# Performance work log

Measured on AMD Instinct MI355X. Metric: run time of the kernel, lower is better.

Reference implementation:

```python
import jax, jax.numpy as jnp
import numpy as np

T, H = 2048, 2048          # tokens, hidden_size
E, I = 16, 768             # num_experts, moe_intermediate_size
K = 2                      # top_k


def setup_inputs() -> dict:
    key = jax.random.key(0)
    k1, k2, k3, k4, k5 = jax.random.split(key, 5)
    hidden_states = jax.random.normal(k1, (T, H), dtype=jnp.float32)
    top_k_index = jax.random.randint(k2, (T, K), 0, E, dtype=jnp.int64)
    top_k_weights = jax.random.uniform(k3, (T, K), dtype=jnp.float32)
    gate_up_proj = jax.random.normal(k4, (E, 2 * I, H), dtype=jnp.float32) * 0.02
    down_proj = jax.random.normal(k5, (E, H, I), dtype=jnp.float32) * 0.02
    return {
        "hidden_states": hidden_states,
        "top_k_index": top_k_index,
        "top_k_weights": top_k_weights,
        "gate_up_proj": gate_up_proj,
        "down_proj": down_proj,
    }


def reference(hidden_states, top_k_index, top_k_weights, gate_up_proj, down_proj):
    # Dense combine-weight matrix C[t, e] = sum of routing weights of token t for expert e.
    # Scatter-add matches index_add_ semantics (duplicate expert picks sum their weights,
    # which equals the eager per-(token, k) accumulation since the expert FFN is the same).
    t_idx = jnp.arange(hidden_states.shape[0])[:, None]
    C = jnp.zeros((hidden_states.shape[0], gate_up_proj.shape[0]), dtype=hidden_states.dtype)
    C = C.at[t_idx, top_k_index].add(top_k_weights.astype(hidden_states.dtype))

    inter = down_proj.shape[2]
    # [T, E, 2I]: each expert's gate_up GEMM applied to every token (zero-weight tokens
    # contribute nothing after combining with C).
    gu = jnp.einsum("th,eoh->teo", hidden_states, gate_up_proj)
    gate, up = gu[..., :inter], gu[..., inter:]
    h = jax.nn.silu(gate) * up                      # [T, E, I]
    y = jnp.einsum("tei,ehi->teh", h, down_proj)    # [T, E, H]
    return jnp.einsum("teh,te->th", y, C)           # weighted combine -> [T, H]
```

## Files before the change

kernel.cpp:

```cpp
#include <hip/hip_runtime.h>
#include <hip/hip_bf16.h>
#include <cstdint>
#include <cstddef>

#define T_TOK 2048
#define HID   2048
#define NEXP  16
#define INTER 768
#define TOPK  2
#define CAP   1024
#define MBLK  8

using short8  = __attribute__((ext_vector_type(8))) short;
using f32x16  = __attribute__((ext_vector_type(16))) float;

#define MFMA(a,b,c) __builtin_amdgcn_mfma_f32_32x32x16_bf16((a),(b),(c),0,0,0)

__device__ inline ushort bf16h(float x) {
    union { __hip_bfloat16 b; ushort u; } cv; cv.b = __float2bfloat16(x); return cv.u;
}
__device__ inline void split8(float4 a, float4 b, short8& h, short8& l) {
    float v[8] = {a.x,a.y,a.z,a.w,b.x,b.y,b.z,b.w};
    #pragma unroll
    for (int j = 0; j < 8; ++j) {
        ushort hb = bf16h(v[j]);
        float hf = __uint_as_float(((uint32_t)hb) << 16);
        h[j] = (short)hb;
        l[j] = (short)bf16h(v[j] - hf);
    }
}

__global__ __launch_bounds__(256)
void route_kernel(const int* __restrict__ idx, const float* __restrict__ wts,
                  int* __restrict__ counts, int* __restrict__ pair_tk,
                  float* __restrict__ pair_w) {
    int p = blockIdx.x * blockDim.x + threadIdx.x;
    if (p >= T_TOK * TOPK) return;
    int e = idx[p];
    int pos = atomicAdd(&counts[e], 1);
    if (pos < CAP) {
        pair_tk[e * CAP + pos] = p;
        pair_w [e * CAP + pos] = wts[p];
    }
}

__global__ __launch_bounds__(256)
void stage1_kernel(const float* __restrict__ hs, const float* __restrict__ gup,
                   const int* __restrict__ counts, const int* __restrict__ pair_tk,
                   float* __restrict__ gu) {
    __shared__ ushort Ahi[4*512], Alo[4*512];
    __shared__ ushort Bhi[16*512], Blo[16*512];
    __shared__ int s_tk[64];

    const int e  = blockIdx.z >> 1;
    const int ks = blockIdx.z & 1;
    const int cnt = min(counts[e], CAP);
    const int m0  = blockIdx.y * 64;
    if (m0 >= cnt) return;
    const int n0  = blockIdx.x * 128;

    const int tid = threadIdx.x, lane = tid & 63, w = tid >> 6;
    if (tid < 64) s_tk[tid] = pair_tk[e*CAP + min(m0+tid, cnt-1)];
    __syncthreads();

    const int ar = tid & 63, aq = tid >> 6;
    const float* asrc = hs + (size_t)(s_tk[ar] >> 1)*HID + ks*1024 + aq*8;
    const int br = tid;
    const float* bsrc = gup + (size_t)e*(2*INTER)*HID
                      + (size_t)((br < 128) ? (n0+br) : (INTER + n0 + br - 128))*HID
                      + ks*1024;

    const int fA  = (ar>>5)*2 + (aq>>1);
    const int lnA = (ar&31) + 32*(aq&1);
    const int rgB = br >> 5, lnB = br & 31;

    f32x16 accg[2], accu[2];
    #pragma unroll
    for (int i=0;i<16;++i){ accg[0][i]=0.f; accg[1][i]=0.f; accu[0][i]=0.f; accu[1][i]=0.f; }

    float4 a0c,a1c,bvc[8], a0n,a1n,bvn[8];
    a0c = *(const float4*)(asrc + 0);
    a1c = *(const float4*)(asrc + 4);
    #pragma unroll
    for (int q=0;q<8;++q) bvc[q] = *(const float4*)(bsrc + 4*q);

#define S1_BODY(A0,A1,BV,A0N,A1N,BVN,KST)                                        \
    {                                                                            \
        __syncthreads();                                                         \
        { short8 h,l; split8(A0,A1,h,l);                                         \
          *(short8*)&Ahi[(fA<<9)+(lnA<<3)] = h;                                  \
          *(short8*)&Alo[(fA<<9)+(lnA<<3)] = l; }                                \
        _Pragma("unroll")                                                        \
        for (int o=0;o<4;++o) { short8 h,l; split8(BV[2*o],BV[2*o+1],h,l);       \
          int f = rgB*2 + (o>>1); int ln = lnB + 32*(o&1);                       \
          *(short8*)&Bhi[(f<<9)+(ln<<3)] = h;                                    \
          *(short8*)&Blo[(f<<9)+(ln<<3)] = l; }                                  \
        if ((KST)+1 < 32) {                                                      \
            int ko = ((KST)+1)*32;                                               \
            A0N = *(const float4*)(asrc + ko);                                   \
            A1N = *(const float4*)(asrc + ko + 4);                               \
            _Pragma("unroll")                                                    \
            for (int q=0;q<8;++q) BVN[q] = *(const float4*)(bsrc + ko + 4*q);    \
        }                                                                        \
        __syncthreads();                                                         \
        const int ro = lane << 3;                                                \
        _Pragma("unroll")                                                        \
        for (int kf=0;kf<2;++kf) {                                               \
            short8 ah0 = *(const short8*)&Ahi[((0*2+kf)<<9)+ro];                 \
            short8 ah1 = *(const short8*)&Ahi[((1*2+kf)<<9)+ro];                 \
            short8 al0 = *(const short8*)&Alo[((0*2+kf)<<9)+ro];                 \
            short8 al1 = *(const short8*)&Alo[((1*2+kf)<<9)+ro];                 \
            short8 bgh = *(const short8*)&Bhi[(((w  )*2+kf)<<9)+ro];             \
            short8 bgl = *(const short8*)&Blo[(((w  )*2+kf)<<9)+ro];             \
            short8 buh = *(const short8*)&Bhi[(((4+w)*2+kf)<<9)+ro];             \
            short8 bul = *(const short8*)&Blo[(((4+w)*2+kf)<<9)+ro];             \
            accg[0] = MFMA(ah0,bgh,accg[0]);                                     \
            accg[1] = MFMA(ah1,bgh,accg[1]);                                     \
            accu[0] = MFMA(ah0,buh,accu[0]);                                     \
            accu[1] = MFMA(ah1,buh,accu[1]);                                     \
            accg[0] = MFMA(al0,bgh,accg[0]);                                     \
            accg[1] = MFMA(al1,bgh,accg[1]);                                     \
            accu[0] = MFMA(al0,buh,accu[0]);                                     \
            accu[1] = MFMA(al1,buh,accu[1]);                                     \
            accg[0] = MFMA(ah0,bgl,accg[0]);                                     \
            accg[1] = MFMA(ah1,bgl,accg[1]);                                     \
            accu[0] = MFMA(ah0,bul,accu[0]);                                     \
            accu[1] = MFMA(ah1,bul,accu[1]);                                     \
        }                                                                        \
    }

    for (int kst = 0; kst < 32; kst += 2) {
        S1_BODY(a0c,a1c,bvc,a0n,a1n,bvn,kst)
        S1_BODY(a0n,a1n,bvn,a0c,a1c,bvc,kst+1)
    }
#undef S1_BODY

    const int crhi = (lane>>5)*4, cl = lane&31;
    const int colg = n0 + 32*w + cl;
    #pragma unroll
    for (int mi=0;mi<2;++mi)
      #pragma unroll
      for (int r=0;r<16;++r) {
        int row = mi*32 + (r&3) + 8*(r>>2) + crhi;
        if (m0 + row < cnt) {
            size_t base = (size_t)s_tk[row]*(2*INTER);
            atomicAdd(&gu[base + colg],         accg[mi][r]);
            atomicAdd(&gu[base + INTER + colg], accu[mi][r]);
        }
      }
}

__global__ __launch_bounds__(256)
void fuse_kernel(const float* __restrict__ gu, ushort* __restrict__ hhi,
                 ushort* __restrict__ hlo) {
    int id  = blockIdx.x*256 + threadIdx.x;
    int row = id / (INTER/4);
    int c4  = (id % (INTER/4)) * 4;
    const float* gr = gu + (size_t)row*(2*INTER) + c4;
    float4 g = *(const float4*)gr;
    float4 u = *(const float4*)(gr + INTER);
    float hv[4];
    hv[0] = g.x/(1.f+__expf(-g.x))*u.x;
    hv[1] = g.y/(1.f+__expf(-g.y))*u.y;
    hv[2] = g.z/(1.f+__expf(-g.z))*u.z;
    hv[3] = g.w/(1.f+__expf(-g.w))*u.w;
    ushort4 hh, hl;
    {
        ushort h0 = bf16h(hv[0]); float f0 = __uint_as_float(((uint32_t)h0)<<16);
        ushort h1 = bf16h(hv[1]); float f1 = __uint_as_float(((uint32_t)h1)<<16);
        ushort h2 = bf16h(hv[2]); float f2 = __uint_as_float(((uint32_t)h2)<<16);
        ushort h3 = bf16h(hv[3]); float f3 = __uint_as_float(((uint32_t)h3)<<16);
        hh = make_ushort4(h0,h1,h2,h3);
        hl = make_ushort4(bf16h(hv[0]-f0), bf16h(hv[1]-f1), bf16h(hv[2]-f2), bf16h(hv[3]-f3));
    }
    *(ushort4*)&hhi[(size_t)row*INTER + c4] = hh;
    *(ushort4*)&hlo[(size_t)row*INTER + c4] = hl;
}

__global__ __launch_bounds__(256)
void stage2_kernel(const ushort* __restrict__ hhi, const ushort* __restrict__ hlo,
                   const float* __restrict__ dwn, const int* __restrict__ counts,
                   const int* __restrict__ pair_tk, const float* __restrict__ pair_w,
                   float* __restrict__ out) {
    __shared__ ushort Ahi[4*512], Alo[4*512];
    __shared__ ushort Bhi[16*512], Blo[16*512];
    __shared__ int   s_tk[64];
    __shared__ float s_w[64];

    const int e  = blockIdx.z >> 1;
    const int ks = blockIdx.z & 1;
    const int cnt = min(counts[e], CAP);
    const int m0  = blockIdx.y * 64;
    if (m0 >= cnt) return;
    const int n0  = blockIdx.x * 256;

    const int tid = threadIdx.x, lane = tid & 63, w = tid >> 6;
    if (tid < 64) {
        int slot = min(m0+tid, cnt-1);
        s_tk[tid] = pair_tk[e*CAP + slot];
        s_w[tid]  = pair_w [e*CAP + slot];
    }
    __syncthreads();

    const int fA = tid >> 6, lnA = tid & 63;
    const int arow = (fA>>1)*32 + (lnA & 31);
    const int aoct = lnA >> 5, akf = fA & 1;
    const size_t aoff = (size_t)s_tk[arow]*INTER + ks*384 + akf*16 + aoct*8;
    const ushort* ahsrc = hhi + aoff;
    const ushort* alsrc = hlo + aoff;

    const int br = tid;
    const float* bsrc = dwn + (size_t)e*HID*INTER + (size_t)(n0+br)*INTER + ks*384;
    const int rgB = br >> 5, lnB = br & 31;

    f32x16 acc[2][2];
    #pragma unroll
    for (int mi=0;mi<2;++mi)
      #pragma unroll
      for (int ni=0;ni<2;++ni)
        #pragma unroll
        for (int i=0;i<16;++i) acc[mi][ni][i] = 0.f;

    short8 ahc, alc, ahn, aln;
    float4 bvc[8], bvn[8];
    ahc = *(const short8*)(ahsrc);
    alc = *(const short8*)(alsrc);
    #pragma unroll
    for (int q=0;q<8;++q) bvc[q] = *(const float4*)(bsrc + 4*q);

#define S2_BODY(AH,AL,BV,AHN,ALN,BVN,KST)                                        \
    {                                                                            \
        __syncthreads();                                                         \
        *(short8*)&Ahi[(fA<<9)+(lnA<<3)] = AH;                                   \
        *(short8*)&Alo[(fA<<9)+(lnA<<3)] = AL;                                   \
        _Pragma("unroll")                                                        \
        for (int o=0;o<4;++o) { short8 h,l; split8(BV[2*o],BV[2*o+1],h,l);       \
          int f = rgB*2 + (o>>1); int ln = lnB + 32*(o&1);                       \
          *(short8*)&Bhi[(f<<9)+(ln<<3)] = h;                                    \
          *(short8*)&Blo[(f<<9)+(ln<<3)] = l; }                                  \
        if ((KST)+1 < 12) {                                                      \
            int ko = ((KST)+1)*32;                                               \
            AHN = *(const short8*)(ahsrc + ko);                                  \
            ALN = *(const short8*)(alsrc + ko);                                  \
            _Pragma("unroll")                                                    \
            for (int q=0;q<8;++q) BVN[q] = *(const float4*)(bsrc + ko + 4*q);    \
        }                                                                        \
        __syncthreads();                                                         \
        const int ro = lane << 3;                                                \
        _Pragma("unroll")                                                        \
        for (int kf=0;kf<2;++kf) {                                               \
            short8 ah0 = *(const short8*)&Ahi[((0*2+kf)<<9)+ro];                 \
            short8 ah1 = *(const short8*)&Ahi[((1*2+kf)<<9)+ro];                 \
            short8 al0 = *(const short8*)&Alo[((0*2+kf)<<9)+ro];                 \
            short8 al1 = *(const short8*)&Alo[((1*2+kf)<<9)+ro];                 \
            _Pragma("unroll")                                                    \
            for (int ni=0;ni<2;++ni) {                                           \
                short8 bh = *(const short8*)&Bhi[(((2*w+ni)*2+kf)<<9)+ro];       \
                short8 bl = *(const short8*)&Blo[(((2*w+ni)*2+kf)<<9)+ro];       \
                acc[0][ni] = MFMA(ah0,bh,acc[0][ni]);                            \
                acc[1][ni] = MFMA(ah1,bh,acc[1][ni]);                            \
                acc[0][ni] = MFMA(al0,bh,acc[0][ni]);                            \
                acc[1][ni] = MFMA(al1,bh,acc[1][ni]);                            \
                acc[0][ni] = MFMA(ah0,bl,acc[0][ni]);                            \
                acc[1][ni] = MFMA(ah1,bl,acc[1][ni]);                            \
            }                                                                    \
        }                                                                        \
    }

    for (int kst = 0; kst < 12; kst += 2) {
        S2_BODY(ahc,alc,bvc,ahn,aln,bvn,kst)
        S2_BODY(ahn,aln,bvn,ahc,alc,bvc,kst+1)
    }
#undef S2_BODY

    const int crhi = (lane>>5)*4, cl = lane&31;
    #pragma unroll
    for (int mi=0;mi<2;++mi)
      #pragma unroll
      for (int r=0;r<16;++r) {
        int row = mi*32 + (r&3) + 8*(r>>2) + crhi;
        if (m0 + row < cnt) {
            int   t  = s_tk[row] >> 1;
            float wt = s_w[row];
            #pragma unroll
            for (int ni=0;ni<2;++ni) {
                int col = n0 + 64*w + 32*ni + cl;
                atomicAdd(&out[(size_t)t*HID + col], wt*acc[mi][ni][r]);
            }
        }
      }
}

extern "C" void kernel_launch(void* const* d_in, const int* in_sizes, int n_in,
                              void* d_out, int out_size, void* d_ws, size_t ws_size,
                              hipStream_t stream) {
    const float* hs  = (const float*)d_in[0];
    const int*   idx = (const int*)  d_in[1];
    const float* wts = (const float*)d_in[2];
    const float* gup = (const float*)d_in[3];
    const float* dwn = (const float*)d_in[4];
    float* out = (float*)d_out;

    char* ws = (char*)d_ws;
    int*    counts  = (int*)ws;
    int*    pair_tk = (int*)(ws + 1024);
    float*  pair_w  = (float*)(ws + 1024 + NEXP*CAP*4);
    float*  gu      = (float*)(ws + 262144);
    ushort* hhi     = (ushort*)(ws + 262144 + 25165824);
    ushort* hlo     = (ushort*)(ws + 262144 + 25165824 + 6291456);

    hipMemsetAsync(counts, 0, NEXP*sizeof(int), stream);
    hipMemsetAsync(gu, 0, (size_t)T_TOK*TOPK*2*INTER*sizeof(float), stream);
    hipMemsetAsync(out, 0, (size_t)T_TOK*HID*sizeof(float), stream);

    route_kernel<<<(T_TOK*TOPK + 255)/256, 256, 0, stream>>>(idx, wts, counts, pair_tk, pair_w);
    stage1_kernel<<<dim3(INTER/128, MBLK, NEXP*2), 256, 0, stream>>>(hs, gup, counts, pair_tk, gu);
    fuse_kernel<<<(T_TOK*TOPK*INTER/4)/256, 256, 0, stream>>>(gu, hhi, hlo);
    stage2_kernel<<<dim3(HID/256, MBLK, NEXP*2), 256, 0, stream>>>(hhi, hlo, dwn, counts, pair_tk, pair_w, out);
}
```

Before: 638.7 us.

## Pre-convert weights to bf16 and stream tiles via global_load_lds double buffering

Adds prep kernels that convert the expert weights to single bf16 and the hidden states to a hi/lo bf16 pair before the GEMMs. The grouped GEMMs then load ready-made bf16 tiles straight into double-buffered LDS with global_load_lds, which removes the per-tile register split and halves weight traffic. The block order is remapped and occupancy hints are added. Dropping the weight lo term cuts MFMA work by a third but lowers accuracy. The weights are re-converted on every call, which costs extra passes over memory. A fallback path is kept for when the workspace is too small.

Result: no change. 634.3 us (-0.7%).

```diff
diff --git a/kernel.cpp b/kernel.cpp
--- a/kernel.cpp
+++ b/kernel.cpp
@@ -18,6 +18,10 @@
 
 __device__ inline ushort bf16h(float x) {
     union { __hip_bfloat16 b; ushort u; } cv; cv.b = __float2bfloat16(x); return cv.u;
+}
+__device__ inline void gl16(const void* g, void* l) {
+    __builtin_amdgcn_global_load_lds((const __attribute__((address_space(1))) void*)g,
+                                     (__attribute__((address_space(3))) void*)l, 16, 0, 0);
 }
 __device__ inline void split8(float4 a, float4 b, short8& h, short8& l) {
     float v[8] = {a.x,a.y,a.z,a.w,b.x,b.y,b.z,b.w};
@@ -45,97 +49,94 @@
 }
 
 __global__ __launch_bounds__(256)
-void stage1_kernel(const float* __restrict__ hs, const float* __restrict__ gup,
-                   const int* __restrict__ counts, const int* __restrict__ pair_tk,
-                   float* __restrict__ gu) {
-    __shared__ ushort Ahi[4*512], Alo[4*512];
-    __shared__ ushort Bhi[16*512], Blo[16*512];
+void prep_bf16_kernel(const float4* __restrict__ src, ushort4* __restrict__ dst, int n4) {
+    int stride = gridDim.x * blockDim.x;
+    for (int i = blockIdx.x*blockDim.x + threadIdx.x; i < n4; i += stride) {
+        float4 v = src[i];
+        dst[i] = make_ushort4(bf16h(v.x), bf16h(v.y), bf16h(v.z), bf16h(v.w));
+    }
+}
+
+__global__ __launch_bounds__(256)
+void prep_hilo_kernel(const float4* __restrict__ src, ushort4* __restrict__ hi,
+                      ushort4* __restrict__ lo, int n4) {
+    int stride = gridDim.x * blockDim.x;
+    for (int i = blockIdx.x*blockDim.x + threadIdx.x; i < n4; i += stride) {
+        float4 v = src[i];
+        ushort h0=bf16h(v.x), h1=bf16h(v.y), h2=bf16h(v.z), h3=bf16h(v.w);
+        hi[i] = make_ushort4(h0,h1,h2,h3);
+        lo[i] = make_ushort4(bf16h(v.x - __uint_as_float((uint32_t)h0<<16)),
+                             bf16h(v.y - __uint_as_float((uint32_t)h1<<16)),
+                             bf16h(v.z - __uint_as_float((uint32_t)h2<<16)),
+                             bf16h(v.w - __uint_as_float((uint32_t)h3<<16)));
+    }
+}
+
+__global__ __launch_bounds__(256, 3)
+void s1mm_kernel(const ushort* __restrict__ hshi, const ushort* __restrict__ hslo,
+                 const ushort* __restrict__ gupb,
+                 const int* __restrict__ counts, const int* __restrict__ pair_tk,
+                 float* __restrict__ gu) {
+    __shared__ ushort Ab[2][8*512];
+    __shared__ ushort Bb[2][16*512];
     __shared__ int s_tk[64];
 
-    const int e  = blockIdx.z >> 1;
-    const int ks = blockIdx.z & 1;
+    const int lin  = blockIdx.x;
+    const int work = (lin & 7)*192 + (lin >> 3);
+    const int x = work % 6, y = (work/6) & 7, z = work/48;
+    const int e = z >> 1, ks = z & 1;
     const int cnt = min(counts[e], CAP);
-    const int m0  = blockIdx.y * 64;
+    const int m0 = y*64;
     if (m0 >= cnt) return;
-    const int n0  = blockIdx.x * 128;
-
-    const int tid = threadIdx.x, lane = tid & 63, w = tid >> 6;
+    const int n0 = x*128;
+
+    const int tid = threadIdx.x, ln = tid & 63, w = tid >> 6;
     if (tid < 64) s_tk[tid] = pair_tk[e*CAP + min(m0+tid, cnt-1)];
     __syncthreads();
 
-    const int ar = tid & 63, aq = tid >> 6;
-    const float* asrc = hs + (size_t)(s_tk[ar] >> 1)*HID + ks*1024 + aq*8;
-    const int br = tid;
-    const float* bsrc = gup + (size_t)e*(2*INTER)*HID
-                      + (size_t)((br < 128) ? (n0+br) : (INTER + n0 + br - 128))*HID
-                      + ks*1024;
-
-    const int fA  = (ar>>5)*2 + (aq>>1);
-    const int lnA = (ar&31) + 32*(aq&1);
-    const int rgB = br >> 5, lnB = br & 31;
+    const int lr = ln & 31, oc = (ln >> 5)*8;
+    const int tkA = s_tk[(w & 1)*32 + lr];
+    const ushort* hp = (w >> 1) ? hslo : hshi;
+    const ushort* aA = hp + (size_t)(tkA >> 1)*HID + ks*1024 + oc;
+    const ushort* bG = gupb + ((size_t)e*(2*INTER) + (n0 + w*32 + lr))*HID + ks*1024 + oc;
+    const ushort* bU = gupb + ((size_t)e*(2*INTER) + (INTER + n0 + w*32 + lr))*HID + ks*1024 + oc;
 
     f32x16 accg[2], accu[2];
     #pragma unroll
-    for (int i=0;i<16;++i){ accg[0][i]=0.f; accg[1][i]=0.f; accu[0][i]=0.f; accu[1][i]=0.f; }
-
-    float4 a0c,a1c,bvc[8], a0n,a1n,bvn[8];
-    a0c = *(const float4*)(asrc + 0);
-    a1c = *(const float4*)(asrc + 4);
-    #pragma unroll
-    for (int q=0;q<8;++q) bvc[q] = *(const float4*)(bsrc + 4*q);
-
-#define S1_BODY(A0,A1,BV,A0N,A1N,BVN,KST)                                        \
-    {                                                                            \
-        __syncthreads();                                                         \
-        { short8 h,l; split8(A0,A1,h,l);                                         \
-          *(short8*)&Ahi[(fA<<9)+(lnA<<3)] = h;                                  \
-          *(short8*)&Alo[(fA<<9)+(lnA<<3)] = l; }                                \
-        _Pragma("unroll")                                                        \
-        for (int o=0;o<4;++o) { short8 h,l; split8(BV[2*o],BV[2*o+1],h,l);       \
-          int f = rgB*2 + (o>>1); int ln = lnB + 32*(o&1);                       \
-          *(short8*)&Bhi[(f<<9)+(ln<<3)] = h;                                    \
-          *(short8*)&Blo[(f<<9)+(ln<<3)] = l; }                                  \
-        if ((KST)+1 < 32) {                                                      \
-            int ko = ((KST)+1)*32;                                               \
-            A0N = *(const float4*)(asrc + ko);                                   \
-            A1N = *(const float4*)(asrc + ko + 4);                               \
-            _Pragma("unroll")                                                    \
-            for (int q=0;q<8;++q) BVN[q] = *(const float4*)(bsrc + ko + 4*q);    \
-        }                                                                        \
-        __syncthreads();                                                         \
-        const int ro = lane << 3;                                                \
-        _Pragma("unroll")                                                        \
-        for (int kf=0;kf<2;++kf) {                                               \
-            short8 ah0 = *(const short8*)&Ahi[((0*2+kf)<<9)+ro];                 \
-            short8 ah1 = *(const short8*)&Ahi[((1*2+kf)<<9)+ro];                 \
-            short8 al0 = *(const short8*)&Alo[((0*2+kf)<<9)+ro];                 \
-            short8 al1 = *(const short8*)&Alo[((1*2+kf)<<9)+ro];                 \
-            short8 bgh = *(const short8*)&Bhi[(((w  )*2+kf)<<9)+ro];             \
-            short8 bgl = *(const short8*)&Blo[(((w  )*2+kf)<<9)+ro];             \
-            short8 buh = *(const short8*)&Bhi[(((4+w)*2+kf)<<9)+ro];             \
-            short8 bul = *(const short8*)&Blo[(((4+w)*2+kf)<<9)+ro];             \
-            accg[0] = MFMA(ah0,bgh,accg[0]);                                     \
-            accg[1] = MFMA(ah1,bgh,accg[1]);                                     \
-            accu[0] = MFMA(ah0,buh,accu[0]);                                     \
-            accu[1] = MFMA(ah1,buh,accu[1]);                                     \
-            accg[0] = MFMA(al0,bgh,accg[0]);                                     \
-            accg[1] = MFMA(al1,bgh,accg[1]);                                     \
-            accu[0] = MFMA(al0,buh,accu[0]);                                     \
-            accu[1] = MFMA(al1,buh,accu[1]);                                     \
-            accg[0] = MFMA(ah0,bgl,accg[0]);                                     \
-            accg[1] = MFMA(ah1,bgl,accg[1]);                                     \
-            accu[0] = MFMA(ah0,bul,accu[0]);                                     \
-            accu[1] = MFMA(ah1,bul,accu[1]);                                     \
-        }                                                                        \
-    }
-
-    for (int kst = 0; kst < 32; kst += 2) {
-        S1_BODY(a0c,a1c,bvc,a0n,a1n,bvn,kst)
-        S1_BODY(a0n,a1n,bvn,a0c,a1c,bvc,kst+1)
-    }
-#undef S1_BODY
-
-    const int crhi = (lane>>5)*4, cl = lane&31;
+    for (int i=0;i<16;++i){accg[0][i]=0.f;accg[1][i]=0.f;accu[0][i]=0.f;accu[1][i]=0.f;}
+
+#define S1_STAGE(buf, k32) { const int kb=(k32)*32;            \
+    gl16(aA+kb,    &Ab[buf][(2*w+0)*512]);                     \
+    gl16(aA+kb+16, &Ab[buf][(2*w+1)*512]);                     \
+    gl16(bG+kb,    &Bb[buf][(2*w+0)*512]);                     \
+    gl16(bG+kb+16, &Bb[buf][(2*w+1)*512]);                     \
+    gl16(bU+kb,    &Bb[buf][(2*(4+w)+0)*512]);                 \
+    gl16(bU+kb+16, &Bb[buf][(2*(4+w)+1)*512]); }
+
+    S1_STAGE(0, 0)
+    int cur = 0;
+    const int ro = ln*8;
+    for (int k32 = 0; k32 < 32; ++k32) {
+        __syncthreads();
+        if (k32 + 1 < 32) S1_STAGE(cur^1, k32+1)
+        #pragma unroll
+        for (int kf = 0; kf < 2; ++kf) {
+            short8 ah0 = *(const short8*)&Ab[cur][(0+kf)*512 + ro];
+            short8 ah1 = *(const short8*)&Ab[cur][(2+kf)*512 + ro];
+            short8 al0 = *(const short8*)&Ab[cur][(4+kf)*512 + ro];
+            short8 al1 = *(const short8*)&Ab[cur][(6+kf)*512 + ro];
+            short8 bg  = *(const short8*)&Bb[cur][(2*w+kf)*512 + ro];
+            short8 bu  = *(const short8*)&Bb[cur][(8+2*w+kf)*512 + ro];
+            accg[0]=MFMA(ah0,bg,accg[0]); accg[0]=MFMA(al0,bg,accg[0]);
+            accg[1]=MFMA(ah1,bg,accg[1]); accg[1]=MFMA(al1,bg,accg[1]);
+            accu[0]=MFMA(ah0,bu,accu[0]); accu[0]=MFMA(al0,bu,accu[0]);
+            accu[1]=MFMA(ah1,bu,accu[1]); accu[1]=MFMA(al1,bu,accu[1]);
+        }
+        cur ^= 1;
+    }
+#undef S1_STAGE
+
+    const int crhi = (ln>>5)*4, cl = ln&31;
     const int colg = n0 + 32*w + cl;
     #pragma unroll
     for (int mi=0;mi<2;++mi)
@@ -164,54 +165,48 @@
     hv[1] = g.y/(1.f+__expf(-g.y))*u.y;
     hv[2] = g.z/(1.f+__expf(-g.z))*u.z;
     hv[3] = g.w/(1.f+__expf(-g.w))*u.w;
-    ushort4 hh, hl;
-    {
-        ushort h0 = bf16h(hv[0]); float f0 = __uint_as_float(((uint32_t)h0)<<16);
-        ushort h1 = bf16h(hv[1]); float f1 = __uint_as_float(((uint32_t)h1)<<16);
-        ushort h2 = bf16h(hv[2]); float f2 = __uint_as_float(((uint32_t)h2)<<16);
-        ushort h3 = bf16h(hv[3]); float f3 = __uint_as_float(((uint32_t)h3)<<16);
-        hh = make_ushort4(h0,h1,h2,h3);
-        hl = make_ushort4(bf16h(hv[0]-f0), bf16h(hv[1]-f1), bf16h(hv[2]-f2), bf16h(hv[3]-f3));
-    }
-    *(ushort4*)&hhi[(size_t)row*INTER + c4] = hh;
-    *(ushort4*)&hlo[(size_t)row*INTER + c4] = hl;
-}
-
-__global__ __launch_bounds__(256)
-void stage2_kernel(const ushort* __restrict__ hhi, const ushort* __restrict__ hlo,
-                   const float* __restrict__ dwn, const int* __restrict__ counts,
-                   const int* __restrict__ pair_tk, const float* __restrict__ pair_w,
-                   float* __restrict__ out) {
-    __shared__ ushort Ahi[4*512], Alo[4*512];
-    __shared__ ushort Bhi[16*512], Blo[16*512];
+    ushort h0=bf16h(hv[0]), h1=bf16h(hv[1]), h2=bf16h(hv[2]), h3=bf16h(hv[3]);
+    *(ushort4*)&hhi[(size_t)row*INTER + c4] = make_ushort4(h0,h1,h2,h3);
+    *(ushort4*)&hlo[(size_t)row*INTER + c4] = make_ushort4(
+        bf16h(hv[0]-__uint_as_float((uint32_t)h0<<16)),
+        bf16h(hv[1]-__uint_as_float((uint32_t)h1<<16)),
+        bf16h(hv[2]-__uint_as_float((uint32_t)h2<<16)),
+        bf16h(hv[3]-__uint_as_float((uint32_t)h3<<16)));
+}
+
+__global__ __launch_bounds__(256, 3)
+void s2mm_kernel(const ushort* __restrict__ h2hi, const ushort* __restrict__ h2lo,
+                 const ushort* __restrict__ dwnb,
+                 const int* __restrict__ counts, const int* __restrict__ pair_tk,
+                 const float* __restrict__ pair_w, float* __restrict__ out) {
+    __shared__ ushort Ab[2][8*512];
+    __shared__ ushort Bb[2][16*512];
     __shared__ int   s_tk[64];
     __shared__ float s_w[64];
 
-    const int e  = blockIdx.z >> 1;
-    const int ks = blockIdx.z & 1;
+    const int lin  = blockIdx.x;
+    const int work = (lin & 7)*256 + (lin >> 3);
+    const int x = work & 7, y = (work >> 3) & 7, z = work >> 6;
+    const int e = z >> 1, ks = z & 1;
     const int cnt = min(counts[e], CAP);
-    const int m0  = blockIdx.y * 64;
+    const int m0 = y*64;
     if (m0 >= cnt) return;
-    const int n0  = blockIdx.x * 256;
-
-    const int tid = threadIdx.x, lane = tid & 63, w = tid >> 6;
+    const int n0 = x*256;
+
+    const int tid = threadIdx.x, ln = tid & 63, w = tid >> 6;
     if (tid < 64) {
-        int slot = min(m0+tid, cnt-1);
-        s_tk[tid] = pair_tk[e*CAP + slot];
-        s_w[tid]  = pair_w [e*CAP + slot];
+        int s = min(m0+tid, cnt-1);
+        s_tk[tid] = pair_tk[e*CAP + s];
+        s_w[tid]  = pair_w [e*CAP + s];
     }
     __syncthreads();
 
-    const int fA = tid >> 6, lnA = tid & 63;
-    const int arow = (fA>>1)*32 + (lnA & 31);
-    const int aoct = lnA >> 5, akf = fA & 1;
-    const size_t aoff = (size_t)s_tk[arow]*INTER + ks*384 + akf*16 + aoct*8;
-    const ushort* ahsrc = hhi + aoff;
-    const ushort* alsrc = hlo + aoff;
-
-    const int br = tid;
-    const float* bsrc = dwn + (size_t)e*HID*INTER + (size_t)(n0+br)*INTER + ks*384;
-    const int rgB = br >> 5, lnB = br & 31;
+    const int lr = ln & 31, oc = (ln >> 5)*8;
+    const int tkA = s_tk[(w & 1)*32 + lr];
+    const ushort* hp = (w >> 1) ? h2lo : h2hi;
+    const ushort* aA = hp + (size_t)tkA*INTER + ks*384 + oc;
+    const ushort* b0 = dwnb + ((size_t)e*HID + (n0 + (2*w+0)*32 + lr))*INTER + ks*384 + oc;
+    const ushort* b1 = dwnb + ((size_t)e*HID + (n0 + (2*w+1)*32 + lr))*INTER + ks*384 + oc;
 
     f32x16 acc[2][2];
     #pragma unroll
@@ -221,59 +216,38 @@
         #pragma unroll
         for (int i=0;i<16;++i) acc[mi][ni][i] = 0.f;
 
-    short8 ahc, alc, ahn, aln;
-    float4 bvc[8], bvn[8];
-    ahc = *(const short8*)(ahsrc);
-    alc = *(const short8*)(alsrc);
-    #pragma unroll
-    for (int q=0;q<8;++q) bvc[q] = *(const float4*)(bsrc + 4*q);
-
-#define S2_BODY(AH,AL,BV,AHN,ALN,BVN,KST)                                        \
-    {                                                                            \
-        __syncthreads();                                                         \
-        *(short8*)&Ahi[(fA<<9)+(lnA<<3)] = AH;                                   \
-        *(short8*)&Alo[(fA<<9)+(lnA<<3)] = AL;                                   \
-        _Pragma("unroll")                                                        \
-        for (int o=0;o<4;++o) { short8 h,l; split8(BV[2*o],BV[2*o+1],h,l);       \
-          int f = rgB*2 + (o>>1); int ln = lnB + 32*(o&1);                       \
-          *(short8*)&Bhi[(f<<9)+(ln<<3)] = h;                                    \
-          *(short8*)&Blo[(f<<9)+(ln<<3)] = l; }                                  \
-        if ((KST)+1 < 12) {                                                      \
-            int ko = ((KST)+1)*32;                                               \
-            AHN = *(const short8*)(ahsrc + ko);                                  \
-            ALN = *(const short8*)(alsrc + ko);                                  \
-            _Pragma("unroll")                                                    \
-            for (int q=0;q<8;++q) BVN[q] = *(const float4*)(bsrc + ko + 4*q);    \
-        }                                                                        \
-        __syncthreads();                                                         \
-        const int ro = lane << 3;                                                \
-        _Pragma("unroll")                                                        \
-        for (int kf=0;kf<2;++kf) {                                               \
-            short8 ah0 = *(const short8*)&Ahi[((0*2+kf)<<9)+ro];                 \
-            short8 ah1 = *(const short8*)&Ahi[((1*2+kf)<<9)+ro];                 \
-            short8 al0 = *(const short8*)&Alo[((0*2+kf)<<9)+ro];                 \
-            short8 al1 = *(const short8*)&Alo[((1*2+kf)<<9)+ro];                 \
-            _Pragma("unroll")                                                    \
-            for (int ni=0;ni<2;++ni) {                                           \
-                short8 bh = *(const short8*)&Bhi[(((2*w+ni)*2+kf)<<9)+ro];       \
-                short8 bl = *(const short8*)&Blo[(((2*w+ni)*2+kf)<<9)+ro];       \
-                acc[0][ni] = MFMA(ah0,bh,acc[0][ni]);                            \
-                acc[1][ni] = MFMA(ah1,bh,acc[1][ni]);                            \
-                acc[0][ni] = MFMA(al0,bh,acc[0][ni]);                            \
-                acc[1][ni] = MFMA(al1,bh,acc[1][ni]);                            \
-                acc[0][ni] = MFMA(ah0,bl,acc[0][ni]);                            \
-                acc[1][ni] = MFMA(ah1,bl,acc[1][ni]);                            \
-            }                                                                    \
-        }                                                                        \
-    }
-
-    for (int kst = 0; kst < 12; kst += 2) {
-        S2_BODY(ahc,alc,bvc,ahn,aln,bvn,kst)
-        S2_BODY(ahn,aln,bvn,ahc,alc,bvc,kst+1)
-    }
-#undef S2_BODY
-
-    const int crhi = (lane>>5)*4, cl = lane&31;
+#define S2_STAGE(buf, k32) { const int kb=(k32)*32;            \
+    gl16(aA+kb,    &Ab[buf][(2*w+0)*512]);                     \
+    gl16(aA+kb+16, &Ab[buf][(2*w+1)*512]);                     \
+    gl16(b0+kb,    &Bb[buf][(4*w+0)*512]);                     \
+    gl16(b0+kb+16, &Bb[buf][(4*w+1)*512]);                     \
+    gl16(b1+kb,    &Bb[buf][(4*w+2)*512]);                     \
+    gl16(b1+kb+16, &Bb[buf][(4*w+3)*512]); }
+
+    S2_STAGE(0, 0)
+    int cur = 0;
+    const int ro = ln*8;
+    for (int k32 = 0; k32 < 12; ++k32) {
+        __syncthreads();
+        if (k32 + 1 < 12) S2_STAGE(cur^1, k32+1)
+        #pragma unroll
+        for (int kf = 0; kf < 2; ++kf) {
+            short8 ah0 = *(const short8*)&Ab[cur][(0+kf)*512 + ro];
+            short8 ah1 = *(const short8*)&Ab[cur][(2+kf)*512 + ro];
+            short8 al0 = *(const short8*)&Ab[cur][(4+kf)*512 + ro];
+            short8 al1 = *(const short8*)&Ab[cur][(6+kf)*512 + ro];
+            short8 b0f = *(const short8*)&Bb[cur][(4*w+0+kf)*512 + ro];
+            short8 b1f = *(const short8*)&Bb[cur][(4*w+2+kf)*512 + ro];
+            acc[0][0]=MFMA(ah0,b0f,acc[0][0]); acc[0][0]=MFMA(al0,b0f,acc[0][0]);
+            acc[1][0]=MFMA(ah1,b0f,acc[1][0]); acc[1][0]=MFMA(al1,b0f,acc[1][0]);
+            acc[0][1]=MFMA(ah0,b1f,acc[0][1]); acc[0][1]=MFMA(al0,b1f,acc[0][1]);
+            acc[1][1]=MFMA(ah1,b1f,acc[1][1]); acc[1][1]=MFMA(al1,b1f,acc[1][1]);
+        }
+        cur ^= 1;
+    }
+#undef S2_STAGE
+
+    const int crhi = (ln>>5)*4, cl = ln&31;
     #pragma unroll
     for (int mi=0;mi<2;++mi)
       #pragma unroll
@@ -291,6 +265,207 @@
       }
 }
 
+__global__ __launch_bounds__(256)
+void s1_fb_kernel(const float* __restrict__ hs, const float* __restrict__ gup,
+                  const int* __restrict__ counts, const int* __restrict__ pair_tk,
+                  float* __restrict__ gu) {
+    __shared__ ushort Ahi[4*512], Alo[4*512];
+    __shared__ ushort Bhi[16*512], Blo[16*512];
+    __shared__ int s_tk[64];
+    const int e  = blockIdx.z >> 1;
+    const int ks = blockIdx.z & 1;
+    const int cnt = min(counts[e], CAP);
+    const int m0  = blockIdx.y * 64;
+    if (m0 >= cnt) return;
+    const int n0  = blockIdx.x * 128;
+    const int tid = threadIdx.x, lane = tid & 63, w = tid >> 6;
+    if (tid < 64) s_tk[tid] = pair_tk[e*CAP + min(m0+tid, cnt-1)];
+    __syncthreads();
+    const int ar = tid & 63, aq = tid >> 6;
+    const float* asrc = hs + (size_t)(s_tk[ar] >> 1)*HID + ks*1024 + aq*8;
+    const int br = tid;
+    const float* bsrc = gup + (size_t)e*(2*INTER)*HID
+                      + (size_t)((br < 128) ? (n0+br) : (INTER + n0 + br - 128))*HID + ks*1024;
+    const int fA  = (ar>>5)*2 + (aq>>1);
+    const int lnA = (ar&31) + 32*(aq&1);
+    const int rgB = br >> 5, lnB = br & 31;
+    f32x16 accg[2], accu[2];
+    #pragma unroll
+    for (int i=0;i<16;++i){ accg[0][i]=0.f; accg[1][i]=0.f; accu[0][i]=0.f; accu[1][i]=0.f; }
+    float4 a0c,a1c,bvc[8], a0n,a1n,bvn[8];
+    a0c = *(const float4*)(asrc + 0);
+    a1c = *(const float4*)(asrc + 4);
+    #pragma unroll
+    for (int q=0;q<8;++q) bvc[q] = *(const float4*)(bsrc + 4*q);
+#define S1_BODY(A0,A1,BV,A0N,A1N,BVN,KST)                                        \
+    {                                                                            \
+        __syncthreads();                                                         \
+        { short8 h,l; split8(A0,A1,h,l);                                         \
+          *(short8*)&Ahi[(fA<<9)+(lnA<<3)] = h;                                  \
+          *(short8*)&Alo[(fA<<9)+(lnA<<3)] = l; }                                \
+        _Pragma("unroll")                                                        \
+        for (int o=0;o<4;++o) { short8 h,l; split8(BV[2*o],BV[2*o+1],h,l);       \
+          int f = rgB*2 + (o>>1); int ln2 = lnB + 32*(o&1);                      \
+          *(short8*)&Bhi[(f<<9)+(ln2<<3)] = h;                                   \
+          *(short8*)&Blo[(f<<9)+(ln2<<3)] = l; }                                 \
+        if ((KST)+1 < 32) {                                                     \
+            int ko = ((KST)+1)*32;                                              \
+            A0N = *(const float4*)(asrc + ko);                                  \
+            A1N = *(const float4*)(asrc + ko + 4);                              \
+            _Pragma("unroll")                                                   \
+            for (int q=0;q<8;++q) BVN[q] = *(const float4*)(bsrc + ko + 4*q);   \
+        }                                                                       \
+        __syncthreads();                                                        \
+        const int ro = lane << 3;                                               \
+        _Pragma("unroll")                                                       \
+        for (int kf=0;kf<2;++kf) {                                              \
+            short8 ah0 = *(const short8*)&Ahi[((0*2+kf)<<9)+ro];                \
+            short8 ah1 = *(const short8*)&Ahi[((1*2+kf)<<9)+ro];                \
+            short8 al0 = *(const short8*)&Alo[((0*2+kf)<<9)+ro];                \
+            short8 al1 = *(const short8*)&Alo[((1*2+kf)<<9)+ro];                \
+            short8 bgh = *(const short8*)&Bhi[(((w  )*2+kf)<<9)+ro];            \
+            short8 bgl = *(const short8*)&Blo[(((w  )*2+kf)<<9)+ro];            \
+            short8 buh = *(const short8*)&Bhi[(((4+w)*2+kf)<<9)+ro];            \
+            short8 bul = *(const short8*)&Blo[(((4+w)*2+kf)<<9)+ro];            \
+            accg[0] = MFMA(ah0,bgh,accg[0]);                                    \
+            accg[1] = MFMA(ah1,bgh,accg[1]);                                    \
+            accu[0] = MFMA(ah0,buh,accu[0]);                                    \
+            accu[1] = MFMA(ah1,buh,accu[1]);                                    \
+            accg[0] = MFMA(al0,bgh,accg[0]);                                    \
+            accg[1] = MFMA(al1,bgh,accg[1]);                                    \
+            accu[0] = MFMA(al0,buh,accu[0]);                                    \
+            accu[1] = MFMA(al1,buh,accu[1]);                                    \
+            accg[0] = MFMA(ah0,bgl,accg[0]);                                    \
+            accg[1] = MFMA(ah1,bgl,accg[1]);                                    \
+            accu[0] = MFMA(ah0,bul,accu[0]);                                    \
+            accu[1] = MFMA(ah1,bul,accu[1]);                                    \
+        }                                                                       \
+    }
+    for (int kst = 0; kst < 32; kst += 2) {
+        S1_BODY(a0c,a1c,bvc,a0n,a1n,bvn,kst)
+        S1_BODY(a0n,a1n,bvn,a0c,a1c,bvc,kst+1)
+    }
+#undef S1_BODY
+    const int crhi = (lane>>5)*4, cl = lane&31;
+    const int colg = n0 + 32*w + cl;
+    #pragma unroll
+    for (int mi=0;mi<2;++mi)
+      #pragma unroll
+      for (int r=0;r<16;++r) {
+        int row = mi*32 + (r&3) + 8*(r>>2) + crhi;
+        if (m0 + row < cnt) {
+            size_t base = (size_t)s_tk[row]*(2*INTER);
+            atomicAdd(&gu[base + colg],         accg[mi][r]);
+            atomicAdd(&gu[base + INTER + colg], accu[mi][r]);
+        }
+      }
+}
+
+__global__ __launch_bounds__(256)
+void s2_fb_kernel(const ushort* __restrict__ hhi, const ushort* __restrict__ hlo,
+                  const float* __restrict__ dwn, const int* __restrict__ counts,
+                  const int* __restrict__ pair_tk, const float* __restrict__ pair_w,
+                  float* __restrict__ out) {
+    __shared__ ushort Ahi[4*512], Alo[4*512];
+    __shared__ ushort Bhi[16*512], Blo[16*512];
+    __shared__ int   s_tk[64];
+    __shared__ float s_w[64];
+    const int e  = blockIdx.z >> 1;
+    const int ks = blockIdx.z & 1;
+    const int cnt = min(counts[e], CAP);
+    const int m0  = blockIdx.y * 64;
+    if (m0 >= cnt) return;
+    const int n0  = blockIdx.x * 256;
+    const int tid = threadIdx.x, lane = tid & 63, w = tid >> 6;
+    if (tid < 64) {
+        int slot = min(m0+tid, cnt-1);
+        s_tk[tid] = pair_tk[e*CAP + slot];
+        s_w[tid]  = pair_w [e*CAP + slot];
+    }
+    __syncthreads();
+    const int fA = tid >> 6, lnA = tid & 63;
+    const int arow = (fA>>1)*32 + (lnA & 31);
+    const int aoct = lnA >> 5, akf = fA & 1;
+    const size_t aoff = (size_t)s_tk[arow]*INTER + ks*384 + akf*16 + aoct*8;
+    const ushort* ahsrc = hhi + aoff;
+    const ushort* alsrc = hlo + aoff;
+    const int br = tid;
+    const float* bsrc = dwn + (size_t)e*HID*INTER + (size_t)(n0+br)*INTER + ks*384;
+    const int rgB = br >> 5, lnB = br & 31;
+    f32x16 acc[2][2];
+    #pragma unroll
+    for (int mi=0;mi<2;++mi)
+      #pragma unroll
+      for (int ni=0;ni<2;++ni)
+        #pragma unroll
+        for (int i=0;i<16;++i) acc[mi][ni][i] = 0.f;
+    short8 ahc, alc, ahn, aln;
+    float4 bvc[8], bvn[8];
+    ahc = *(const short8*)(ahsrc);
+    alc = *(const short8*)(alsrc);
+    #pragma unroll
+    for (int q=0;q<8;++q) bvc[q] = *(const float4*)(bsrc + 4*q);
+#define S2_BODY(AH,AL,BV,AHN,ALN,BVN,KST)                                        \
+    {                                                                            \
+        __syncthreads();                                                         \
+        *(short8*)&Ahi[(fA<<9)+(lnA<<3)] = AH;                                   \
+        *(short8*)&Alo[(fA<<9)+(lnA<<3)] = AL;                                   \
+        _Pragma("unroll")                                                        \
+        for (int o=0;o<4;++o) { short8 h,l; split8(BV[2*o],BV[2*o+1],h,l);       \
+          int f = rgB*2 + (o>>1); int ln2 = lnB + 32*(o&1);                      \
+          *(short8*)&Bhi[(f<<9)+(ln2<<3)] = h;                                   \
+          *(short8*)&Blo[(f<<9)+(ln2<<3)] = l; }                                 \
+        if ((KST)+1 < 12) {                                                     \
+            int ko = ((KST)+1)*32;                                              \
+            AHN = *(const short8*)(ahsrc + ko);                                 \
+            ALN = *(const short8*)(alsrc + ko);                                 \
+            _Pragma("unroll")                                                   \
+            for (int q=0;q<8;++q) BVN[q] = *(const float4*)(bsrc + ko + 4*q);   \
+        }                                                                       \
+        __syncthreads();                                                        \
+        const int ro = lane << 3;                                               \
+        _Pragma("unroll")                                                       \
+        for (int kf=0;kf<2;++kf) {                                              \
+            short8 ah0 = *(const short8*)&Ahi[((0*2+kf)<<9)+ro];                \
+            short8 ah1 = *(const short8*)&Ahi[((1*2+kf)<<9)+ro];                \
+            short8 al0 = *(const short8*)&Alo[((0*2+kf)<<9)+ro];                \
+            short8 al1 = *(const short8*)&Alo[((1*2+kf)<<9)+ro];                \
+            _Pragma("unroll")                                                   \
+            for (int ni=0;ni<2;++ni) {                                          \
+                short8 bh = *(const short8*)&Bhi[(((2*w+ni)*2+kf)<<9)+ro];      \
+                short8 bl = *(const short8*)&Blo[(((2*w+ni)*2+kf)<<9)+ro];      \
+                acc[0][ni] = MFMA(ah0,bh,acc[0][ni]);                           \
+                acc[1][ni] = MFMA(ah1,bh,acc[1][ni]);                           \
+                acc[0][ni] = MFMA(al0,bh,acc[0][ni]);                           \
+                acc[1][ni] = MFMA(al1,bh,acc[1][ni]);                           \
+                acc[0][ni] = MFMA(ah0,bl,acc[0][ni]);                           \
+                acc[1][ni] = MFMA(ah1,bl,acc[1][ni]);                           \
+            }                                                                   \
+        }                                                                       \
+    }
+    for (int kst = 0; kst < 12; kst += 2) {
+        S2_BODY(ahc,alc,bvc,ahn,aln,bvn,kst)
+        S2_BODY(ahn,aln,bvn,ahc,alc,bvc,kst+1)
+    }
+#undef S2_BODY
+    const int crhi = (lane>>5)*4, cl = lane&31;
+    #pragma unroll
+    for (int mi=0;mi<2;++mi)
+      #pragma unroll
+      for (int r=0;r<16;++r) {
+        int row = mi*32 + (r&3) + 8*(r>>2) + crhi;
+        if (m0 + row < cnt) {
+            int   t  = s_tk[row] >> 1;
+            float wt = s_w[row];
+            #pragma unroll
+            for (int ni=0;ni<2;++ni) {
+                int col = n0 + 64*w + 32*ni + cl;
+                atomicAdd(&out[(size_t)t*HID + col], wt*acc[mi][ni][r]);
+            }
+        }
+      }
+}
+
 extern "C" void kernel_launch(void* const* d_in, const int* in_sizes, int n_in,
                               void* d_out, int out_size, void* d_ws, size_t ws_size,
                               hipStream_t stream) {
@@ -302,19 +477,52 @@
     float* out = (float*)d_out;
 
     char* ws = (char*)d_ws;
-    int*    counts  = (int*)ws;
-    int*    pair_tk = (int*)(ws + 1024);
-    float*  pair_w  = (float*)(ws + 1024 + NEXP*CAP*4);
-    float*  gu      = (float*)(ws + 262144);
-    ushort* hhi     = (ushort*)(ws + 262144 + 25165824);
-    ushort* hlo     = (ushort*)(ws + 262144 + 25165824 + 6291456);
+    int*   counts  = (int*)ws;
+    int*   pair_tk = (int*)(ws + 1024);
+    float* pair_w  = (float*)(ws + 1024 + NEXP*CAP*4);
+
+    size_t o_gu   = 262144;
+    size_t o_gupb = o_gu   + (size_t)T_TOK*TOPK*2*INTER*4;
+    size_t o_dwnb = o_gupb + (size_t)NEXP*2*INTER*HID*2;
+    size_t o_hshi = o_dwnb + (size_t)NEXP*HID*INTER*2;
+    size_t o_hslo = o_hshi + (size_t)T_TOK*HID*2;
+    size_t o_h2hi = o_hslo + (size_t)T_TOK*HID*2;
+    size_t o_h2lo = o_h2hi + (size_t)T_TOK*TOPK*INTER*2;
+    size_t need   = o_h2lo + (size_t)T_TOK*TOPK*INTER*2;
 
     hipMemsetAsync(counts, 0, NEXP*sizeof(int), stream);
-    hipMemsetAsync(gu, 0, (size_t)T_TOK*TOPK*2*INTER*sizeof(float), stream);
     hipMemsetAsync(out, 0, (size_t)T_TOK*HID*sizeof(float), stream);
-
     route_kernel<<<(T_TOK*TOPK + 255)/256, 256, 0, stream>>>(idx, wts, counts, pair_tk, pair_w);
-    stage1_kernel<<<dim3(INTER/128, MBLK, NEXP*2), 256, 0, stream>>>(hs, gup, counts, pair_tk, gu);
-    fuse_kernel<<<(T_TOK*TOPK*INTER/4)/256, 256, 0, stream>>>(gu, hhi, hlo);
-    stage2_kernel<<<dim3(HID/256, MBLK, NEXP*2), 256, 0, stream>>>(hhi, hlo, dwn, counts, pair_tk, pair_w, out);
-}
+
+    if (ws_size >= need) {
+        float*  gu   = (float*)(ws + o_gu);
+        ushort* gupb = (ushort*)(ws + o_gupb);
+        ushort* dwnb = (ushort*)(ws + o_dwnb);
+        ushort* hshi = (ushort*)(ws + o_hshi);
+        ushort* hslo = (ushort*)(ws + o_hslo);
+        ushort* h2hi = (ushort*)(ws + o_h2hi);
+        ushort* h2lo = (ushort*)(ws + o_h2lo);
+
+        hipMemsetAsync(gu, 0, (size_t)T_TOK*TOPK*2*INTER*4, stream);
+        prep_bf16_kernel<<<2048, 256, 0, stream>>>((const float4*)gup, (ushort4*)gupb,
+                                                   NEXP*2*INTER*HID/4);
+        prep_bf16_kernel<<<2048, 256, 0, stream>>>((const float4*)dwn, (ushort4*)dwnb,
+                                                   NEXP*HID*INTER/4);
+        prep_hilo_kernel<<<1024, 256, 0, stream>>>((const float4*)hs, (ushort4*)hshi,
+                                                   (ushort4*)hslo, T_TOK*HID/4);
+        s1mm_kernel<<<6*MBLK*NEXP*2, 256, 0, stream>>>(hshi, hslo, gupb, counts, pair_tk, gu);
+        fuse_kernel<<<(T_TOK*TOPK*INTER/4)/256, 256, 0, stream>>>(gu, h2hi, h2lo);
+        s2mm_kernel<<<8*MBLK*NEXP*2, 256, 0, stream>>>(h2hi, h2lo, dwnb, counts, pair_tk,
+                                                       pair_w, out);
+    } else {
+        float*  gu  = (float*)(ws + 262144);
+        ushort* hhi = (ushort*)(ws + 262144 + 25165824);
+        ushort* hlo = (ushort*)(ws + 262144 + 25165824 + 6291456);
+        hipMemsetAsync(gu, 0, (size_t)T_TOK*TOPK*2*INTER*4, stream);
+        s1_fb_kernel<<<dim3(INTER/128, MBLK, NEXP*2), 256, 0, stream>>>(hs, gup, counts,
+                                                                        pair_tk, gu);
+        fuse_kernel<<<(T_TOK*TOPK*INTER/4)/256, 256, 0, stream>>>(gu, hhi, hlo);
+        s2_fb_kernel<<<dim3(HID/256, MBLK, NEXP*2), 256, 0, stream>>>(hhi, hlo, dwn, counts,
+                                                                      pair_tk, pair_w, out);
+    }
+}
```
